# Kernel optimization log

Hardware: AMD Instinct MI355X
Metric: run time of the kernel (lower is better)

Reference implementation:

```python
import jax, jax.numpy as jnp
import numpy as np

B_, T_, IN_, OUT_, N_ = 16, 4096, 512, 512, 512


def setup_inputs() -> dict:
    key = jax.random.key(0)
    ks = jax.random.split(key, 9)
    u = jax.random.normal(ks[0], (B_, T_, IN_), dtype=jnp.float32)
    # LRU init per original module
    rmin, rmax, max_phase = 0.9, 1.0, 6.283
    u1 = jax.random.uniform(ks[1], (N_,), dtype=jnp.float32)
    u2 = jax.random.uniform(ks[2], (N_,), dtype=jnp.float32)
    nu_log = jnp.log(-0.5 * jnp.log(u1 * (rmax + rmin) * (rmax - rmin) + rmin ** 2))
    theta_log = jnp.log(max_phase * u2)
    Lambda_mod = jnp.exp(-jnp.exp(nu_log))
    gamma_log = jnp.log(jnp.sqrt(1.0 - jnp.square(Lambda_mod)))
    B_re = jax.random.normal(ks[3], (N_, IN_), dtype=jnp.float32) / np.sqrt(2 * IN_)
    B_im = jax.random.normal(ks[4], (N_, IN_), dtype=jnp.float32) / np.sqrt(2 * IN_)
    C_re = jax.random.normal(ks[5], (OUT_, N_), dtype=jnp.float32) / np.sqrt(N_)
    C_im = jax.random.normal(ks[6], (OUT_, N_), dtype=jnp.float32) / np.sqrt(N_)
    D = jax.random.normal(ks[7], (OUT_, IN_), dtype=jnp.float32) / np.sqrt(IN_)
    return {"u": u, "nu_log": nu_log, "theta_log": theta_log, "gamma_log": gamma_log,
            "B_re": B_re, "B_im": B_im, "C_re": C_re, "C_im": C_im, "D": D}


def reference(u, nu_log, theta_log, gamma_log, B_re, B_im, C_re, C_im, D):
    # Lambda: diagonal complex transition, |Lambda| = exp(-exp(nu_log)), angle = exp(theta_log)
    mod = jnp.exp(-jnp.exp(nu_log))             # [N]
    theta = jnp.exp(theta_log)
    Lam = jax.lax.complex(mod * jnp.cos(theta), mod * jnp.sin(theta))  # [N] complex64
    gammas = jnp.exp(gamma_log)                  # [N]
    Bc = jax.lax.complex(B_re, B_im) * gammas[:, None]                 # [N, IN]
    Cc = jax.lax.complex(C_re, C_im)                                   # [OUT, N]

    # input projection: Bu[b,t,n] = sum_i Bc[n,i] * u[b,t,i]
    Bu = jnp.einsum('bti,ni->btn', u.astype(Bc.dtype), Bc)             # [B,T,N] complex

    # diagonal linear recurrence x_t = Lam * x_{t-1} + Bu_t, state starts at 0
    a = jnp.broadcast_to(Lam, Bu.shape)

    def combine(e1, e2):
        a1, b1 = e1
        a2, b2 = e2
        return a1 * a2, a2 * b1 + b2

    _, x = jax.lax.associative_scan(combine, (a, Bu), axis=1)          # x: [B,T,N]

    y = 2.0 * jnp.einsum('btn,on->bto', x, Cc).real + jnp.einsum('bti,oi->bto', u, D)
    return y
```

## Files before the change

kernel.cpp:

```cpp
#include <hip/hip_runtime.h>
#include <hip/hip_bf16.h>
#include <cstdint>
#include <cstddef>


using short8 = __attribute__((ext_vector_type(8))) short;
using f32x4 = __attribute__((ext_vector_type(4))) float;

#define BDIM 16
#define TDIM 4096
#define MTOT (BDIM * TDIM)
#define CHUNK 64
#define NCHUNK (TDIM / CHUNK)

__device__ __forceinline__ unsigned short f2bf(float f) {
    unsigned u = __float_as_uint(f);
    u = u + 0x7FFFu + ((u >> 16) & 1u);
    return (unsigned short)(u >> 16);
}
__device__ __forceinline__ float bflo(unsigned w) { return __uint_as_float(w << 16); }
__device__ __forceinline__ float bfhi(unsigned w) { return __uint_as_float(w & 0xFFFF0000u); }

__device__ __forceinline__ size_t perm_off(int row, int kt, int kp, int rowbytes) {
    int kk = kp >> 5, km = kp & 31;
    int half = km >> 4;
    int g = (km & 15) >> 2, j = km & 3;
    int cc = (kk << 2) | g;
    int c = cc ^ (row & 7);
    return (size_t)row * rowbytes + kt * 128 + (c << 4) + half * 8 + j * 2;
}

__device__ __forceinline__ void gload_lds16(const void* g, void* l) {
    __builtin_amdgcn_global_load_lds((const __attribute__((address_space(1))) void*)g,
                                     (__attribute__((address_space(3))) void*)l, 16, 0, 0);
}

__global__ void prep_w1(const float* __restrict__ B_re, const float* __restrict__ B_im,
                        const float* __restrict__ gamma_log, char* __restrict__ W1) {
    int i = blockIdx.x * 256 + threadIdx.x;
    int r = blockIdx.y;
    int n = r >> 1;
    float gmm = expf(gamma_log[n]);
    float v = (r & 1) ? B_im[n * 512 + i] * gmm : B_re[n * 512 + i] * gmm;
    *(unsigned short*)(W1 + perm_off(r, i >> 6, i & 63, 1024)) = f2bf(v);
}

__global__ void prep_w2(const float* __restrict__ C_re, const float* __restrict__ C_im,
                        const float* __restrict__ D, char* __restrict__ W2) {
    int k = blockIdx.x * 256 + threadIdx.x;
    int o = blockIdx.y;
    float v;
    if (k < 1024) {
        int n = k >> 1;
        v = (k & 1) ? -2.0f * C_im[o * 512 + n] : 2.0f * C_re[o * 512 + n];
    } else {
        v = D[o * 512 + (k - 1024)];
    }
    *(unsigned short*)(W2 + perm_off(o, k >> 6, k & 63, 3072)) = f2bf(v);
}

__global__ void convert_u(const float4* __restrict__ u4, char* __restrict__ Apack) {
    size_t idx = (size_t)blockIdx.x * 256 + threadIdx.x;
    float4 v = u4[idx];
    int row = (int)(idx >> 7);
    int c4 = (int)(idx & 127);
    int kg = 1024 + c4 * 4;
    unsigned lo = (unsigned)f2bf(v.x) | ((unsigned)f2bf(v.y) << 16);
    unsigned hi = (unsigned)f2bf(v.z) | ((unsigned)f2bf(v.w) << 16);
    size_t off = perm_off(row, kg >> 6, kg & 63, 3072);
    *reinterpret_cast<uint2*>(Apack + off) = make_uint2(lo, hi);
}

#define ASM_VMCNT4 asm volatile("s_waitcnt vmcnt(4)" ::: "memory")
#define ASM_VMCNT0 asm volatile("s_waitcnt vmcnt(0)" ::: "memory")
#define ASM_LGKM0  asm volatile("s_waitcnt lgkmcnt(0)" ::: "memory")
#define SCHED0     __builtin_amdgcn_sched_barrier(0)
#define BARRIER    __builtin_amdgcn_s_barrier()
#define PRIO1      __builtin_amdgcn_s_setprio(1)
#define PRIO0      __builtin_amdgcn_s_setprio(0)

template <int OUT_MODE, int NBN>
__global__ __launch_bounds__(512, 2) void gemm_nt(const char* __restrict__ A, int ldab,
                                                  const char* __restrict__ Bm, int ldbb,
                                                  void* __restrict__ Cout, int ktiles,
                                                  float2* __restrict__ carry,
                                                  const float* __restrict__ nu_log,
                                                  const float* __restrict__ theta_log) {
    __shared__ __align__(16) char lds[131072];
    const int tid = threadIdx.x;
    const int lane = tid & 63, w = tid >> 6;
    const int bid = blockIdx.x;
    const int cpx = gridDim.x >> 3;
    const int swz = (bid & 7) * cpx + (bid >> 3);
    const int bm = swz / NBN, bn = swz % NBN;
    const int wm = (w >> 2) * 128, wn = (w & 3) * 64;
    const int ml = lane & 15, g = lane >> 4;

    const char* AgrL = A + (size_t)(bm * 256 + w * 16 + (lane >> 3)) * ldab + (lane & 7) * 16;
    const char* BgrL = Bm + (size_t)(bn * 256 + w * 16 + (lane >> 3)) * ldbb + (lane & 7) * 16;

#define STG_A(h, kt_, q) do {                                                         \
        const char* s_ = AgrL + (size_t)((h) * 128) * ldab + (size_t)(kt_) * 128;     \
        char* d_ = lds + (q) * 65536 + (h) * 16384 + w * 2048;                        \
        gload_lds16(s_, d_);                                                          \
        gload_lds16(s_ + (size_t)8 * ldab, d_ + 1024);                                \
    } while (0)
#define STG_B(h, kt_, q) do {                                                         \
        const char* s_ = BgrL + (size_t)((h) * 128) * ldbb + (size_t)(kt_) * 128;     \
        char* d_ = lds + (q) * 65536 + 32768 + (h) * 16384 + w * 2048;                \
        gload_lds16(s_, d_);                                                          \
        gload_lds16(s_ + (size_t)8 * ldbb, d_ + 1024);                                \
    } while (0)

#define RD_A_(mh, Abase) do {                                                         \
        _Pragma("unroll") for (int mt = 0; mt < 4; ++mt)                              \
        _Pragma("unroll") for (int kk = 0; kk < 2; ++kk) {                            \
            int r_ = wm + (mh) * 64 + mt * 16 + ml;                                   \
            int hf_ = r_ >> 7, rl_ = r_ & 127;                                        \
            afr[mt][kk] = *reinterpret_cast<const short8*>(                           \
                (Abase) + hf_ * 16384 + rl_ * 128 + ((((kk << 2) | g) ^ (rl_ & 7)) << 4)); \
        } } while (0)
#define RD_B_(nh, Bbase) do {                                                         \
        _Pragma("unroll") for (int nt = 0; nt < 2; ++nt)                              \
        _Pragma("unroll") for (int kk = 0; kk < 2; ++kk) {                            \
            int c_ = wn + (nh) * 32 + nt * 16 + ml;                                   \
            int hf_ = c_ >> 7, cl_ = c_ & 127;                                        \
            bfr[nh][nt][kk] = *reinterpret_cast<const short8*>(                       \
                (Bbase) + hf_ * 16384 + cl_ * 128 + ((((kk << 2) | g) ^ (cl_ & 7)) << 4)); \
        } } while (0)

#define MFMA16(mh, nh)                                                                \
    _Pragma("unroll") for (int kk = 0; kk < 2; ++kk)                                  \
    _Pragma("unroll") for (int mt = 0; mt < 4; ++mt)                                  \
    _Pragma("unroll") for (int nt = 0; nt < 2; ++nt)                                  \
        acc[(mh) * 4 + mt][(nh) * 2 + nt] = __builtin_amdgcn_mfma_f32_16x16x32_bf16(  \
            afr[mt][kk], bfr[nh][nt][kk], acc[(mh) * 4 + mt][(nh) * 2 + nt], 0, 0, 0)

    f32x4 acc[8][4] = {};
    short8 afr[4][2];
    short8 bfr[2][2][2];

    const char* A0b = lds;
    const char* B0b = lds + 32768;
    const char* A1b = lds + 65536;
    const char* B1b = lds + 98304;

    STG_A(0, 0, 0); STG_A(1, 0, 0); STG_B(0, 0, 0); STG_B(1, 0, 0);
    STG_B(0, 1, 1); STG_B(1, 1, 1);
    ASM_VMCNT4;
    BARRIER;

    const int NT = ktiles >> 1;
    for (int it = 0; it < NT; ++it) {
        const int t1i = 2 * it + 1, t2i = 2 * it + 2, t3i = 2 * it + 3;
        const bool more = (t2i < ktiles);
        RD_A_(0, A0b); RD_B_(0, B0b);
        STG_A(0, t1i, 1);
        BARRIER; ASM_LGKM0; SCHED0;
        PRIO1; MFMA16(0, 0); PRIO0;
        BARRIER;
        RD_B_(1, B0b);
        STG_A(1, t1i, 1);
        BARRIER; ASM_LGKM0; SCHED0;
        PRIO1; MFMA16(0, 1); PRIO0;
        BARRIER;
        RD_A_(1, A0b);
        if (more) STG_B(0, t2i, 0);
        BARRIER; ASM_LGKM0; SCHED0;
        PRIO1; MFMA16(1, 0); PRIO0;
        BARRIER;
        if (more) STG_B(1, t2i, 0);
        PRIO1; MFMA16(1, 1); PRIO0;
        if (more) { ASM_VMCNT4; } else { ASM_VMCNT0; }
        BARRIER;
        RD_A_(0, A1b); RD_B_(0, B1b);
        if (more) STG_A(0, t2i, 0);
        BARRIER; ASM_LGKM0; SCHED0;
        PRIO1; MFMA16(0, 0); PRIO0;
        BARRIER;
        RD_B_(1, B1b);
        if (more) STG_A(1, t2i, 0);
        BARRIER; ASM_LGKM0; SCHED0;
        PRIO1; MFMA16(0, 1); PRIO0;
        BARRIER;
        RD_A_(1, A1b);
        if (more) STG_B(0, t3i, 1);
        BARRIER; ASM_LGKM0; SCHED0;
        PRIO1; MFMA16(1, 0); PRIO0;
        BARRIER;
        if (more) STG_B(1, t3i, 1);
        PRIO1; MFMA16(1, 1); PRIO0;
        if (more) { ASM_VMCNT4; }
        BARRIER;
    }

    if (OUT_MODE == 0) {
        float* O = (float*)Cout;
#pragma unroll
        for (int mt = 0; mt < 8; ++mt)
#pragma unroll
            for (int nt = 0; nt < 4; ++nt)
#pragma unroll
                for (int r_ = 0; r_ < 4; ++r_) {
                    int grow = bm * 256 + wm + mt * 16 + g * 4 + r_;
                    int gcol = bn * 256 + wn + nt * 16 + ml;
                    O[(size_t)grow * 512 + gcol] = acc[mt][nt][r_];
                }
    } else {
        unsigned short* BuOut = (unsigned short*)Cout;
#pragma unroll
        for (int mt = 0; mt < 8; ++mt)
#pragma unroll
            for (int nt = 0; nt < 4; ++nt)
#pragma unroll
                for (int r_ = 0; r_ < 4; ++r_) {
                    int lrow = wm + mt * 16 + g * 4 + r_;
                    int lcol = wn + nt * 16 + ml;
                    unsigned short hv = f2bf(acc[mt][nt][r_]);
                    *(unsigned short*)(lds + lrow * 512 + lcol * 2) = hv;
                    BuOut[(size_t)(bm * 256 + lrow) * 1024 + bn * 256 + lcol] = hv;
                }
        ASM_LGKM0;
        BARRIER;
        SCHED0;
        int n_local = tid & 127, c_local = tid >> 7;
        int nglob = bn * 128 + n_local;
        float mod = expf(-expf(nu_log[nglob]));
        float th = expf(theta_log[nglob]);
        float s, co;
        sincosf(th, &s, &co);
        float Lre = mod * co, Lim = mod * s;
        const char* base = lds + (c_local * 64) * 512 + n_local * 4;
        float xr = 0.f, xi = 0.f;
#pragma unroll 8
        for (int t = 0; t < 64; ++t) {
            unsigned wv = *reinterpret_cast<const unsigned*>(base + t * 512);
            float nr = fmaf(Lre, xr, fmaf(-Lim, xi, bflo(wv)));
            float ni = fmaf(Lre, xi, fmaf(Lim, xr, bfhi(wv)));
            xr = nr; xi = ni;
        }
        int b = (bm * 256) >> 12;
        int cglob = (((bm * 256) & 4095) >> 6) + c_local;
        carry[(size_t)(b * NCHUNK + cglob) * 512 + nglob] = make_float2(xr, xi);
    }
#undef STG_A
#undef STG_B
#undef RD_A_
#undef RD_B_
#undef MFMA16
}

__global__ void scan_prefix(const float2* __restrict__ carry, const float* __restrict__ nu_log,
                            const float* __restrict__ theta_log, float2* __restrict__ prefix) {
    int q = blockIdx.x * 256 + threadIdx.x;
    int n = q & 511, b = q >> 9;
    float e = expf(nu_log[n]);
    float modL = expf(-(float)CHUNK * e);
    float th = expf(theta_log[n]);
    double ang = fmod((double)CHUNK * (double)th, 6.283185307179586);
    float s, co;
    sincosf((float)ang, &s, &co);
    float Lre = modL * co, Lim = modL * s;
    float pr = 0.f, pi = 0.f;
    for (int c = 0; c < NCHUNK; ++c) {
        size_t idx = (size_t)(b * NCHUNK + c) * 512 + n;
        prefix[idx] = make_float2(pr, pi);
        float2 ev = carry[idx];
        float nr = fmaf(Lre, pr, fmaf(-Lim, pi, ev.x));
        float ni = fmaf(Lre, pi, fmaf(Lim, pr, ev.y));
        pr = nr; pi = ni;
    }
}

__global__ void scan_apply(const unsigned* __restrict__ Bu, const float* __restrict__ nu_log,
                           const float* __restrict__ theta_log, const float2* __restrict__ prefix,
                           char* __restrict__ Apack) {
    int q = blockIdx.x * 256 + threadIdx.x;
    int n = q & 511, c = (q >> 9) & 63, b = q >> 15;
    float mod = expf(-expf(nu_log[n]));
    float th = expf(theta_log[n]);
    float s, co;
    sincosf(th, &s, &co);
    float Lre = mod * co, Lim = mod * s;
    const unsigned* p = Bu + ((size_t)(b * TDIM + c * CHUNK)) * 512 + n;
    float2 pv = prefix[(size_t)(b * NCHUNK + c) * 512 + n];
    float xr = pv.x, xi = pv.y;
    int kp = (2 * n) & 63;
    int kk = kp >> 5, km = kp & 31;
    int half = km >> 4, gg = (km & 15) >> 2, j = km & 3;
    int cc = (kk << 2) | gg;
    int partial = (n >> 5) * 128 + half * 8 + j * 2;
    int row0 = b * TDIM + c * CHUNK;
#pragma unroll 8
    for (int t = 0; t < CHUNK; ++t) {
        unsigned wv = p[(size_t)t * 512];
        float nr = fmaf(Lre, xr, fmaf(-Lim, xi, bflo(wv)));
        float ni = fmaf(Lre, xi, fmaf(Lim, xr, bfhi(wv)));
        xr = nr; xi = ni;
        int row = row0 + t;
        size_t off = (size_t)row * 3072 + ((cc ^ (row & 7)) << 4) + partial;
        *reinterpret_cast<unsigned*>(Apack + off) =
            (unsigned)f2bf(xr) | ((unsigned)f2bf(xi) << 16);
    }
}

extern "C" void kernel_launch(void* const* d_in, const int* in_sizes, int n_in,
                              void* d_out, int out_size, void* d_ws, size_t ws_size,
                              hipStream_t stream) {
    const float* u         = (const float*)d_in[0];
    const float* nu_log    = (const float*)d_in[1];
    const float* theta_log = (const float*)d_in[2];
    const float* gamma_log = (const float*)d_in[3];
    const float* B_re      = (const float*)d_in[4];
    const float* B_im      = (const float*)d_in[5];
    const float* C_re      = (const float*)d_in[6];
    const float* C_im      = (const float*)d_in[7];
    const float* D         = (const float*)d_in[8];

    char* ws = (char*)d_ws;
    char* Apack = ws;
    size_t off = (size_t)MTOT * 3072;
    char* W1 = ws + off; off += 1024 * 1024;
    char* W2 = ws + off; off += 512 * 3072;
    float2* carry  = (float2*)(ws + off); off += (size_t)BDIM * NCHUNK * 512 * 8;
    float2* prefix = (float2*)(ws + off); off += (size_t)BDIM * NCHUNK * 512 * 8;

    unsigned short* Bu = (unsigned short*)d_out;

    prep_w1<<<dim3(2, 1024), 256, 0, stream>>>(B_re, B_im, gamma_log, W1);
    prep_w2<<<dim3(6, 512), 256, 0, stream>>>(C_re, C_im, D, W2);
    convert_u<<<32768, 256, 0, stream>>>((const float4*)u, Apack);
    gemm_nt<1, 4><<<1024, 512, 0, stream>>>(Apack + 16 * 128, 3072, W1, 1024,
                                            (void*)Bu, 8, carry, nu_log, theta_log);
    scan_prefix<<<32, 256, 0, stream>>>(carry, nu_log, theta_log, prefix);
    scan_apply<<<2048, 256, 0, stream>>>((const unsigned*)Bu, nu_log, theta_log, prefix, Apack);
    gemm_nt<0, 2><<<512, 512, 0, stream>>>(Apack, 3072, W2, 3072, d_out, 24,
                                           nullptr, nullptr, nullptr);
}
```

Before: 294.7 us.

## Double-buffer A fragments and overlap LDS reads with MFMA via partial lgkmcnt waits

Splits the A register fragments into two banks so the next half-tile's A/B fragments can be read from LDS while MFMAs on the current fragments run. Full lgkmcnt(0) waits become partial lgkmcnt(4/8) waits, and the first fragment reads of each buffer are prefetched across the loop boundary. Several barriers are removed or merged. This raises register pressure and relies on hand-counted LDS wait counts being correct for the reordered issue sequence.

After: 377.5 us. +28.1%, slower.

```diff
diff --git a/kernel.cpp b/kernel.cpp
--- a/kernel.cpp
+++ b/kernel.cpp
@@ -74,6 +74,8 @@
 #define ASM_VMCNT4 asm volatile("s_waitcnt vmcnt(4)" ::: "memory")
 #define ASM_VMCNT0 asm volatile("s_waitcnt vmcnt(0)" ::: "memory")
 #define ASM_LGKM0  asm volatile("s_waitcnt lgkmcnt(0)" ::: "memory")
+#define ASM_LGKM4  asm volatile("s_waitcnt lgkmcnt(4)" ::: "memory")
+#define ASM_LGKM8  asm volatile("s_waitcnt lgkmcnt(8)" ::: "memory")
 #define SCHED0     __builtin_amdgcn_sched_barrier(0)
 #define BARRIER    __builtin_amdgcn_s_barrier()
 #define PRIO1      __builtin_amdgcn_s_setprio(1)
@@ -112,12 +114,12 @@
         gload_lds16(s_ + (size_t)8 * ldbb, d_ + 1024);                                \
     } while (0)
 
-#define RD_A_(mh, Abase) do {                                                         \
+#define RD_A_(bank, Abase) do {                                                       \
         _Pragma("unroll") for (int mt = 0; mt < 4; ++mt)                              \
         _Pragma("unroll") for (int kk = 0; kk < 2; ++kk) {                            \
-            int r_ = wm + (mh) * 64 + mt * 16 + ml;                                   \
+            int r_ = wm + (bank) * 64 + mt * 16 + ml;                                 \
             int hf_ = r_ >> 7, rl_ = r_ & 127;                                        \
-            afr[mt][kk] = *reinterpret_cast<const short8*>(                           \
+            afr[bank][mt][kk] = *reinterpret_cast<const short8*>(                     \
                 (Abase) + hf_ * 16384 + rl_ * 128 + ((((kk << 2) | g) ^ (rl_ & 7)) << 4)); \
         } } while (0)
 #define RD_B_(nh, Bbase) do {                                                         \
@@ -134,10 +136,10 @@
     _Pragma("unroll") for (int mt = 0; mt < 4; ++mt)                                  \
     _Pragma("unroll") for (int nt = 0; nt < 2; ++nt)                                  \
         acc[(mh) * 4 + mt][(nh) * 2 + nt] = __builtin_amdgcn_mfma_f32_16x16x32_bf16(  \
-            afr[mt][kk], bfr[nh][nt][kk], acc[(mh) * 4 + mt][(nh) * 2 + nt], 0, 0, 0)
+            afr[mh][mt][kk], bfr[nh][nt][kk], acc[(mh) * 4 + mt][(nh) * 2 + nt], 0, 0, 0)
 
     f32x4 acc[8][4] = {};
-    short8 afr[4][2];
+    short8 afr[2][4][2];
     short8 bfr[2][2][2];
 
     const char* A0b = lds;
@@ -149,49 +151,49 @@
     STG_B(0, 1, 1); STG_B(1, 1, 1);
     ASM_VMCNT4;
     BARRIER;
+    RD_A_(0, A0b); RD_B_(0, B0b);
 
     const int NT = ktiles >> 1;
     for (int it = 0; it < NT; ++it) {
         const int t1i = 2 * it + 1, t2i = 2 * it + 2, t3i = 2 * it + 3;
         const bool more = (t2i < ktiles);
+        STG_A(0, t1i, 1);
+        BARRIER;
+        RD_B_(1, B0b);
+        ASM_LGKM4; SCHED0;
+        PRIO1; MFMA16(0, 0); PRIO0;
+        STG_A(1, t1i, 1);
+        BARRIER;
+        RD_A_(1, A0b);
+        ASM_LGKM8; SCHED0;
+        PRIO1; MFMA16(0, 1); PRIO0;
+        BARRIER;
+        ASM_LGKM0; SCHED0;
+        PRIO1; MFMA16(1, 0); PRIO0;
+        if (more) { STG_B(0, t2i, 0); STG_B(1, t2i, 0); ASM_VMCNT4; }
+        else      { ASM_VMCNT0; }
+        BARRIER;
+        RD_A_(0, A1b); RD_B_(0, B1b);
+        SCHED0;
+        PRIO1; MFMA16(1, 1); PRIO0;
+        if (more) STG_A(0, t2i, 0);
+        BARRIER;
+        RD_B_(1, B1b);
+        ASM_LGKM4; SCHED0;
+        PRIO1; MFMA16(0, 0); PRIO0;
+        if (more) STG_A(1, t2i, 0);
+        BARRIER;
+        RD_A_(1, A1b);
+        ASM_LGKM8; SCHED0;
+        PRIO1; MFMA16(0, 1); PRIO0;
+        BARRIER;
+        ASM_LGKM0; SCHED0;
+        PRIO1; MFMA16(1, 0); PRIO0;
+        if (more) { STG_B(0, t3i, 1); STG_B(1, t3i, 1); ASM_VMCNT4; }
+        BARRIER;
         RD_A_(0, A0b); RD_B_(0, B0b);
-        STG_A(0, t1i, 1);
-        BARRIER; ASM_LGKM0; SCHED0;
-        PRIO1; MFMA16(0, 0); PRIO0;
-        BARRIER;
-        RD_B_(1, B0b);
-        STG_A(1, t1i, 1);
-        BARRIER; ASM_LGKM0; SCHED0;
-        PRIO1; MFMA16(0, 1); PRIO0;
-        BARRIER;
-        RD_A_(1, A0b);
-        if (more) STG_B(0, t2i, 0);
-        BARRIER; ASM_LGKM0; SCHED0;
-        PRIO1; MFMA16(1, 0); PRIO0;
-        BARRIER;
-        if (more) STG_B(1, t2i, 0);
+        SCHED0;
         PRIO1; MFMA16(1, 1); PRIO0;
-        if (more) { ASM_VMCNT4; } else { ASM_VMCNT0; }
-        BARRIER;
-        RD_A_(0, A1b); RD_B_(0, B1b);
-        if (more) STG_A(0, t2i, 0);
-        BARRIER; ASM_LGKM0; SCHED0;
-        PRIO1; MFMA16(0, 0); PRIO0;
-        BARRIER;
-        RD_B_(1, B1b);
-        if (more) STG_A(1, t2i, 0);
-        BARRIER; ASM_LGKM0; SCHED0;
-        PRIO1; MFMA16(0, 1); PRIO0;
-        BARRIER;
-        RD_A_(1, A1b);
-        if (more) STG_B(0, t3i, 1);
-        BARRIER; ASM_LGKM0; SCHED0;
-        PRIO1; MFMA16(1, 0); PRIO0;
-        BARRIER;
-        if (more) STG_B(1, t3i, 1);
-        PRIO1; MFMA16(1, 1); PRIO0;
-        if (more) { ASM_VMCNT4; }
-        BARRIER;
     }
 
     if (OUT_MODE == 0) {
```

## Reschedule GEMM main loop with deeper prefetch and fewer barriers, template strides

Applied to the files above, without the earlier changes.

Rewrites the software pipeline inside the bf16 MFMA GEMM. The prologue now prefetches an extra A half-tile, and LDS reads for the next B half are issued earlier. Partial lgkmcnt waits let MFMAs start before all fragment loads finish, and several barriers per phase are removed. Row strides become template constants so address arithmetic folds at compile time, and a barrier is added before the epilogue reuses LDS. The aim is to hide global-to-LDS and LDS-to-register latency behind MFMA work, at the cost of a more delicate ordering where a missed wait could race.

Measured after the change: 300.0 us. No clear change (+1.8%).

```diff
diff --git a/kernel.cpp b/kernel.cpp
--- a/kernel.cpp
+++ b/kernel.cpp
@@ -71,17 +71,19 @@
     *reinterpret_cast<uint2*>(Apack + off) = make_uint2(lo, hi);
 }
 
+#define ASM_VMCNT0 asm volatile("s_waitcnt vmcnt(0)" ::: "memory")
 #define ASM_VMCNT4 asm volatile("s_waitcnt vmcnt(4)" ::: "memory")
-#define ASM_VMCNT0 asm volatile("s_waitcnt vmcnt(0)" ::: "memory")
+#define ASM_VMCNT6 asm volatile("s_waitcnt vmcnt(6)" ::: "memory")
 #define ASM_LGKM0  asm volatile("s_waitcnt lgkmcnt(0)" ::: "memory")
+#define ASM_LGKM4  asm volatile("s_waitcnt lgkmcnt(4)" ::: "memory")
 #define SCHED0     __builtin_amdgcn_sched_barrier(0)
 #define BARRIER    __builtin_amdgcn_s_barrier()
 #define PRIO1      __builtin_amdgcn_s_setprio(1)
 #define PRIO0      __builtin_amdgcn_s_setprio(0)
 
-template <int OUT_MODE, int NBN>
-__global__ __launch_bounds__(512, 2) void gemm_nt(const char* __restrict__ A, int ldab,
-                                                  const char* __restrict__ Bm, int ldbb,
+template <int OUT_MODE, int NBN, int LDAB, int LDBB>
+__global__ __launch_bounds__(512, 2) void gemm_nt(const char* __restrict__ A,
+                                                  const char* __restrict__ Bm,
                                                   void* __restrict__ Cout, int ktiles,
                                                   float2* __restrict__ carry,
                                                   const float* __restrict__ nu_log,
@@ -96,26 +98,26 @@
     const int wm = (w >> 2) * 128, wn = (w & 3) * 64;
     const int ml = lane & 15, g = lane >> 4;
 
-    const char* AgrL = A + (size_t)(bm * 256 + w * 16 + (lane >> 3)) * ldab + (lane & 7) * 16;
-    const char* BgrL = Bm + (size_t)(bn * 256 + w * 16 + (lane >> 3)) * ldbb + (lane & 7) * 16;
+    const char* AgrL = A + (size_t)(bm * 256 + w * 16 + (lane >> 3)) * LDAB + (lane & 7) * 16;
+    const char* BgrL = Bm + (size_t)(bn * 256 + w * 16 + (lane >> 3)) * LDBB + (lane & 7) * 16;
 
 #define STG_A(h, kt_, q) do {                                                         \
-        const char* s_ = AgrL + (size_t)((h) * 128) * ldab + (size_t)(kt_) * 128;     \
+        const char* s_ = AgrL + (size_t)((h) * 128) * LDAB + (size_t)(kt_) * 128;     \
         char* d_ = lds + (q) * 65536 + (h) * 16384 + w * 2048;                        \
         gload_lds16(s_, d_);                                                          \
-        gload_lds16(s_ + (size_t)8 * ldab, d_ + 1024);                                \
+        gload_lds16(s_ + (size_t)8 * LDAB, d_ + 1024);                                \
     } while (0)
 #define STG_B(h, kt_, q) do {                                                         \
-        const char* s_ = BgrL + (size_t)((h) * 128) * ldbb + (size_t)(kt_) * 128;     \
+        const char* s_ = BgrL + (size_t)((h) * 128) * LDBB + (size_t)(kt_) * 128;     \
         char* d_ = lds + (q) * 65536 + 32768 + (h) * 16384 + w * 2048;                \
         gload_lds16(s_, d_);                                                          \
-        gload_lds16(s_ + (size_t)8 * ldbb, d_ + 1024);                                \
+        gload_lds16(s_ + (size_t)8 * LDBB, d_ + 1024);                                \
     } while (0)
 
-#define RD_A_(mh, Abase) do {                                                         \
+#define RD_A_(bank, Abase) do {                                                       \
         _Pragma("unroll") for (int mt = 0; mt < 4; ++mt)                              \
         _Pragma("unroll") for (int kk = 0; kk < 2; ++kk) {                            \
-            int r_ = wm + (mh) * 64 + mt * 16 + ml;                                   \
+            int r_ = wm + (bank) * 64 + mt * 16 + ml;                                 \
             int hf_ = r_ >> 7, rl_ = r_ & 127;                                        \
             afr[mt][kk] = *reinterpret_cast<const short8*>(                           \
                 (Abase) + hf_ * 16384 + rl_ * 128 + ((((kk << 2) | g) ^ (rl_ & 7)) << 4)); \
@@ -145,53 +147,56 @@
     const char* A1b = lds + 65536;
     const char* B1b = lds + 98304;
 
-    STG_A(0, 0, 0); STG_A(1, 0, 0); STG_B(0, 0, 0); STG_B(1, 0, 0);
-    STG_B(0, 1, 1); STG_B(1, 1, 1);
-    ASM_VMCNT4;
+    STG_B(0, 0, 0); STG_B(1, 0, 0); STG_A(0, 0, 0); STG_A(1, 0, 0);
+    STG_B(0, 1, 1); STG_B(1, 1, 1); STG_A(0, 1, 1);
+    ASM_VMCNT6;
     BARRIER;
+    SCHED0;
 
     const int NT = ktiles >> 1;
     for (int it = 0; it < NT; ++it) {
         const int t1i = 2 * it + 1, t2i = 2 * it + 2, t3i = 2 * it + 3;
-        const bool more = (t2i < ktiles);
-        RD_A_(0, A0b); RD_B_(0, B0b);
-        STG_A(0, t1i, 1);
-        BARRIER; ASM_LGKM0; SCHED0;
+        const bool more = (it + 1 < NT);
+        RD_B_(0, B0b); RD_A_(0, A0b);
+        SCHED0;
+        RD_B_(1, B0b);
+        BARRIER; SCHED0;
+        STG_A(1, t1i, 1);
+        ASM_LGKM4; SCHED0;
         PRIO1; MFMA16(0, 0); PRIO0;
-        BARRIER;
-        RD_B_(1, B0b);
-        STG_A(1, t1i, 1);
-        BARRIER; ASM_LGKM0; SCHED0;
+        ASM_LGKM0;
+        BARRIER; SCHED0;
+        if (more) STG_B(0, t2i, 0);
         PRIO1; MFMA16(0, 1); PRIO0;
-        BARRIER;
         RD_A_(1, A0b);
-        if (more) STG_B(0, t2i, 0);
-        BARRIER; ASM_LGKM0; SCHED0;
+        BARRIER; SCHED0;
+        if (more) STG_B(1, t2i, 0);
+        ASM_LGKM0; SCHED0;
         PRIO1; MFMA16(1, 0); PRIO0;
-        BARRIER;
-        if (more) STG_B(1, t2i, 0);
+        if (more) { ASM_VMCNT4; } else { ASM_VMCNT0; }
+        BARRIER; SCHED0;
+        if (more) STG_A(0, t2i, 0);
         PRIO1; MFMA16(1, 1); PRIO0;
-        if (more) { ASM_VMCNT4; } else { ASM_VMCNT0; }
-        BARRIER;
-        RD_A_(0, A1b); RD_B_(0, B1b);
-        if (more) STG_A(0, t2i, 0);
-        BARRIER; ASM_LGKM0; SCHED0;
+        RD_B_(0, B1b); RD_A_(0, A1b);
+        SCHED0;
+        RD_B_(1, B1b);
+        BARRIER; SCHED0;
+        if (more) STG_A(1, t2i, 0);
+        ASM_LGKM4; SCHED0;
         PRIO1; MFMA16(0, 0); PRIO0;
-        BARRIER;
-        RD_B_(1, B1b);
-        if (more) STG_A(1, t2i, 0);
-        BARRIER; ASM_LGKM0; SCHED0;
+        ASM_LGKM0;
+        BARRIER; SCHED0;
+        if (more) STG_B(0, t3i, 1);
         PRIO1; MFMA16(0, 1); PRIO0;
-        BARRIER;
         RD_A_(1, A1b);
-        if (more) STG_B(0, t3i, 1);
-        BARRIER; ASM_LGKM0; SCHED0;
+        BARRIER; SCHED0;
+        if (more) STG_B(1, t3i, 1);
+        ASM_LGKM0; SCHED0;
         PRIO1; MFMA16(1, 0); PRIO0;
-        BARRIER;
-        if (more) STG_B(1, t3i, 1);
+        if (more) { ASM_VMCNT4; }
+        BARRIER; SCHED0;
+        if (more) STG_A(0, t3i, 1);
         PRIO1; MFMA16(1, 1); PRIO0;
-        if (more) { ASM_VMCNT4; }
-        BARRIER;
     }
 
     if (OUT_MODE == 0) {
@@ -208,6 +213,7 @@
                 }
     } else {
         unsigned short* BuOut = (unsigned short*)Cout;
+        BARRIER;
 #pragma unroll
         for (int mt = 0; mt < 8; ++mt)
 #pragma unroll
@@ -330,10 +336,10 @@
     prep_w1<<<dim3(2, 1024), 256, 0, stream>>>(B_re, B_im, gamma_log, W1);
     prep_w2<<<dim3(6, 512), 256, 0, stream>>>(C_re, C_im, D, W2);
     convert_u<<<32768, 256, 0, stream>>>((const float4*)u, Apack);
-    gemm_nt<1, 4><<<1024, 512, 0, stream>>>(Apack + 16 * 128, 3072, W1, 1024,
-                                            (void*)Bu, 8, carry, nu_log, theta_log);
+    gemm_nt<1, 4, 3072, 1024><<<1024, 512, 0, stream>>>(Apack + 16 * 128, W1,
+                                                        (void*)Bu, 8, carry, nu_log, theta_log);
     scan_prefix<<<32, 256, 0, stream>>>(carry, nu_log, theta_log, prefix);
     scan_apply<<<2048, 256, 0, stream>>>((const unsigned*)Bu, nu_log, theta_log, prefix, Apack);
-    gemm_nt<0, 2><<<512, 512, 0, stream>>>(Apack, 3072, W2, 3072, d_out, 24,
-                                           nullptr, nullptr, nullptr);
-}
+    gemm_nt<0, 2, 3072, 3072><<<512, 512, 0, stream>>>(Apack, W2, d_out, 24,
+                                                       nullptr, nullptr, nullptr);
+}
```
